# Optimization experiments

Measured on AMD Instinct MI355X. Metric: run time of the kernel, lower is better.

Reference implementation:

```python
import jax, jax.numpy as jnp
import numpy as np

B, S, E = 256, 128, 1024


def setup_inputs() -> dict:
    key = jax.random.key(0)
    k1, k2, k3, k4, k5 = jax.random.split(key, 5)
    x = jax.random.normal(k1, (B, S, E), dtype=jnp.float32)
    # ragged bags: start in [0,32), length in [1,96] so end <= 128 and bags are non-empty
    starts = jax.random.randint(k2, (B,), 0, 32)
    lengths = jax.random.randint(k3, (B,), 1, 97)
    document_index = jnp.stack([starts, starts + lengths], axis=-1).astype(jnp.int32)  # [B,2]
    scale = 1.0 / np.sqrt(E)
    W = jax.random.normal(k4, (E, E), dtype=jnp.float32) * scale  # relationMatrix.weight
    u = jax.random.normal(k5, (1, E), dtype=jnp.float32) * scale  # relationVector.weight
    return {"x": x, "W": W, "u": u, "document_index": document_index}


def reference(x, W, u, document_index):
    # scores_bs = relationVector(tanh(relationMatrix(x)))  (bias-free linears)
    h = jnp.tanh(jnp.einsum('bse,fe->bsf', x, W))          # [B,S,E]
    scores = jnp.einsum('bse,e->bs', h, u[0])              # [B,S]
    # ragged mask: position s belongs to doc b iff start <= s < end
    idx = jnp.arange(S)[None, :]                            # [1,S]
    mask = (idx >= document_index[:, :1]) & (idx < document_index[:, 1:])  # [B,S]
    attn = jax.nn.softmax(jnp.where(mask, scores, -jnp.inf), axis=-1)      # [B,S]
    attn = jnp.where(mask, attn, 0.0)
    out_concat = jnp.einsum('bs,bse->be', attn, x)          # [B,E]
    # keep_attention in the original is the last bag's softmax weights;
    # here returned padded to length S (zeros outside the bag)
    keep_attention = attn[-1]                               # [S]
    return out_concat, keep_attention
```

## Files before the change

kernel.cpp:

```cpp
#include <hip/hip_runtime.h>
#include <math.h>

#define Bb 256
#define Ss 128
#define Ee 1024
#define BK 64
#define APAD 72
#define NMAX 2048

typedef __bf16 bf16x8 __attribute__((ext_vector_type(8)));
typedef float f32x4 __attribute__((ext_vector_type(4)));

typedef __attribute__((address_space(3))) unsigned int lds_u32;
typedef __attribute__((address_space(1))) unsigned int glb_u32;

static __device__ __forceinline__ unsigned short f2bf(float f) {
    unsigned int u = __float_as_uint(f);
    u += 0x7FFFu + ((u >> 16) & 1u);
    return (unsigned short)(u >> 16);
}
static __device__ __forceinline__ float bf2f(unsigned short h) {
    return __uint_as_float((unsigned int)h << 16);
}

__global__ void build_list(const int* __restrict__ doc, int* __restrict__ list) {
    __shared__ int sc[256];
    const int b = threadIdx.x;
    const int start = doc[2 * b], end = doc[2 * b + 1];
    const int s0 = start >> 4;
    const int ns = ((end + 15) >> 4) - s0;
    sc[b] = ns;
    __syncthreads();
    for (int d = 1; d < 256; d <<= 1) {
        int v = sc[b];
        int add = (b >= d) ? sc[b - d] : 0;
        __syncthreads();
        sc[b] = v + add;
        __syncthreads();
    }
    const int total = sc[255];
    const int off = sc[b] - ns;
    for (int i = 0; i < ns; ++i)
        list[off + i] = b * Ss + ((s0 + i) << 4);
    for (int i = total + b; i < NMAX; i += 256)
        list[i] = -1;
}

__global__ void conv_all(const float* __restrict__ x,
                         const float* __restrict__ W,
                         const int* __restrict__ doc,
                         unsigned short* __restrict__ xb,
                         unsigned short* __restrict__ Wb) {
    const int st = blockIdx.x, by = blockIdx.y, tid = threadIdx.x;
    if (by >= Bb) {
        int i = ((((by - Bb) << 3) | st) << 8) | tid;
        float4 v = reinterpret_cast<const float4*>(W)[i];
        ushort4 o;
        o.x = f2bf(v.x); o.y = f2bf(v.y); o.z = f2bf(v.z); o.w = f2bf(v.w);
        reinterpret_cast<ushort4*>(Wb)[i] = o;
        return;
    }
    const int b = by;
    const int start = doc[2 * b], end = doc[2 * b + 1];
    const int strip0 = start >> 4;
    const int ns = ((end + 15) >> 4) - strip0;
    if (st < strip0 || st >= strip0 + ns) return;
    const size_t base = ((size_t)b * Ss + (st << 4)) * Ee;
    #pragma unroll
    for (int r = 0; r < 16; ++r) {
        size_t idx = base + (size_t)r * Ee + (tid << 2);
        float4 v = *reinterpret_cast<const float4*>(x + idx);
        ushort4 o;
        o.x = f2bf(v.x); o.y = f2bf(v.y); o.z = f2bf(v.z); o.w = f2bf(v.w);
        *reinterpret_cast<ushort4*>(xb + idx) = o;
    }
}

__global__ void convW_kernel(const float* __restrict__ W, unsigned short* __restrict__ Wb) {
    int i = blockIdx.x * blockDim.x + threadIdx.x;
    float4 v = reinterpret_cast<const float4*>(W)[i];
    ushort4 o;
    o.x = f2bf(v.x); o.y = f2bf(v.y); o.z = f2bf(v.z); o.w = f2bf(v.w);
    reinterpret_cast<ushort4*>(Wb)[i] = o;
}

__launch_bounds__(256, 6)
__global__ void scores_gemm_xb(const unsigned short* __restrict__ xb,
                               const unsigned short* __restrict__ Wb,
                               const float* __restrict__ u,
                               const int* __restrict__ list,
                               float* __restrict__ part) {
    __shared__ __align__(16) unsigned short As[64 * BK];
    __shared__ __align__(16) unsigned short Bs[128 * BK];
    __shared__ float s_red[4][64];

    const int mb = blockIdx.x;
    const int ft = blockIdx.y;

    int e0 = list[mb << 2];
    if (e0 < 0) return;
    int e[4];
    bool val[4];
    e[0] = e0; val[0] = true;
    #pragma unroll
    for (int j = 1; j < 4; ++j) {
        int v = list[(mb << 2) | j];
        val[j] = v >= 0;
        e[j] = val[j] ? v : e0;
    }

    const int tid  = threadIdx.x;
    const int wave = tid >> 6;
    const int lane = tid & 63;
    const int quad = lane >> 4;
    const int l16  = lane & 15;

    const unsigned short* wbase = Wb + (size_t)ft * 128 * Ee;

    f32x4 acc[4][2];
    #pragma unroll
    for (int i = 0; i < 4; ++i)
        #pragma unroll
        for (int j = 0; j < 2; ++j) acc[i][j] = (f32x4){0.f, 0.f, 0.f, 0.f};

    for (int t = 0; t < 16; ++t) {
        const int k0 = t << 6;
        #pragma unroll
        for (int r = 0; r < 2; ++r) {
            int chunk = (r << 8) | tid;
            int arow = chunk >> 3;
            int strip = arow >> 4;
            int rowin = arow & 15;
            int c8 = (chunk & 7) ^ (arow & 7);
            __builtin_amdgcn_global_load_lds(
                (const glb_u32*)(xb + ((size_t)e[strip] + rowin) * Ee + k0 + (c8 << 3)),
                (lds_u32*)&As[chunk << 3], 16, 0, 0);
        }
        #pragma unroll
        for (int r = 0; r < 4; ++r) {
            int chunk = (r << 8) | tid;
            int brow = chunk >> 3;
            int c8 = (chunk & 7) ^ (brow & 7);
            __builtin_amdgcn_global_load_lds(
                (const glb_u32*)(wbase + (size_t)brow * Ee + k0 + (c8 << 3)),
                (lds_u32*)&Bs[chunk << 3], 16, 0, 0);
        }
        __syncthreads();

        #pragma unroll
        for (int kk = 0; kk < BK; kk += 32) {
            const int n0 = wave * 32 + l16;
            const int n1 = n0 + 16;
            const int c8k = (kk >> 3) + quad;
            bf16x8 bf0 = *reinterpret_cast<const bf16x8*>(
                &Bs[((n0 << 3) | (c8k ^ (n0 & 7))) << 3]);
            bf16x8 bf1 = *reinterpret_cast<const bf16x8*>(
                &Bs[((n1 << 3) | (c8k ^ (n1 & 7))) << 3]);
            #pragma unroll
            for (int st = 0; st < 4; ++st) {
                const int ar = st * 16 + l16;
                bf16x8 af = *reinterpret_cast<const bf16x8*>(
                    &As[((ar << 3) | (c8k ^ (ar & 7))) << 3]);
                acc[st][0] = __builtin_amdgcn_mfma_f32_16x16x32_bf16(af, bf0, acc[st][0], 0, 0, 0);
                acc[st][1] = __builtin_amdgcn_mfma_f32_16x16x32_bf16(af, bf1, acc[st][1], 0, 0, 0);
            }
        }
        __syncthreads();
    }

    const float u0 = u[ft * 128 + wave * 32 + l16];
    const float u1 = u[ft * 128 + wave * 32 + 16 + l16];
    #pragma unroll
    for (int st = 0; st < 4; ++st) {
        float p[4];
        #pragma unroll
        for (int r = 0; r < 4; ++r)
            p[r] = tanhf(acc[st][0][r]) * u0 + tanhf(acc[st][1][r]) * u1;
        #pragma unroll
        for (int off = 8; off >= 1; off >>= 1)
            #pragma unroll
            for (int r = 0; r < 4; ++r)
                p[r] += __shfl_xor(p[r], off, 16);
        if (l16 == 0)
            #pragma unroll
            for (int r = 0; r < 4; ++r)
                s_red[wave][st * 16 + quad * 4 + r] = p[r];
    }
    __syncthreads();
    if (tid < 64) {
        const int strip = tid >> 4;
        if (val[strip]) {
            float v = s_red[0][tid] + s_red[1][tid] + s_red[2][tid] + s_red[3][tid];
            part[((size_t)(e[strip] + (tid & 15)) << 3) | ft] = v;
        }
    }
}

__launch_bounds__(256)
__global__ void scores_gemm_fb(const float* __restrict__ x,
                               const unsigned short* __restrict__ Wb,
                               const float* __restrict__ u,
                               const int* __restrict__ doc,
                               float* __restrict__ part) {
    __shared__ __align__(16) unsigned short As[8 * 16 * APAD];
    __shared__ __align__(16) unsigned short Bs[128 * BK];
    __shared__ float s_red[4][128];

    const int b  = blockIdx.x;
    const int ft = blockIdx.y;
    const int start = doc[2 * b], end = doc[2 * b + 1];
    const int strip0 = start >> 4;
    const int ns = ((end + 15) >> 4) - strip0;
    const int row0 = strip0 << 4;

    const int tid  = threadIdx.x;
    const int wave = tid >> 6;
    const int lane = tid & 63;
    const int quad = lane >> 4;
    const int l16  = lane & 15;
    const int arow = tid >> 4;
    const int acol = (tid & 15) << 2;

    const float* xbase = x + ((size_t)b * Ss + row0) * Ee;
    const unsigned short* wbase = Wb + (size_t)ft * 128 * Ee;

    f32x4 acc[8][2];
    #pragma unroll
    for (int i = 0; i < 8; ++i)
        #pragma unroll
        for (int j = 0; j < 2; ++j) acc[i][j] = (f32x4){0.f, 0.f, 0.f, 0.f};

    for (int k0 = 0; k0 < Ee; k0 += BK) {
        #pragma unroll
        for (int r = 0; r < 8; ++r) if (r < ns) {
            int row = (r << 4) | arow;
            float4 v = *reinterpret_cast<const float4*>(xbase + (size_t)row * Ee + k0 + acol);
            ushort4 o; o.x = f2bf(v.x); o.y = f2bf(v.y); o.z = f2bf(v.z); o.w = f2bf(v.w);
            *reinterpret_cast<ushort4*>(&As[row * APAD + acol]) = o;
        }
        #pragma unroll
        for (int r = 0; r < 4; ++r) {
            int chunk = (r << 8) | tid;
            int brow = chunk >> 3;
            int c8 = (chunk & 7) ^ (brow & 7);
            __builtin_amdgcn_global_load_lds(
                (const glb_u32*)(wbase + (size_t)brow * Ee + k0 + (c8 << 3)),
                (lds_u32*)&Bs[chunk << 3], 16, 0, 0);
        }
        __syncthreads();
        #pragma unroll
        for (int kk = 0; kk < BK; kk += 32) {
            const int n0 = wave * 32 + l16;
            const int n1 = n0 + 16;
            const int c8k = (kk >> 3) + quad;
            bf16x8 bf0 = *reinterpret_cast<const bf16x8*>(
                &Bs[((n0 << 3) | (c8k ^ (n0 & 7))) << 3]);
            bf16x8 bf1 = *reinterpret_cast<const bf16x8*>(
                &Bs[((n1 << 3) | (c8k ^ (n1 & 7))) << 3]);
            #pragma unroll
            for (int st = 0; st < 8; ++st) {
                if (st < ns) {
                    bf16x8 af = *reinterpret_cast<const bf16x8*>(
                        &As[(st * 16 + l16) * APAD + kk + quad * 8]);
                    acc[st][0] = __builtin_amdgcn_mfma_f32_16x16x32_bf16(af, bf0, acc[st][0], 0, 0, 0);
                    acc[st][1] = __builtin_amdgcn_mfma_f32_16x16x32_bf16(af, bf1, acc[st][1], 0, 0, 0);
                }
            }
        }
        __syncthreads();
    }

    const float u0 = u[ft * 128 + wave * 32 + l16];
    const float u1 = u[ft * 128 + wave * 32 + 16 + l16];
    #pragma unroll
    for (int st = 0; st < 8; ++st) {
        if (st < ns) {
            float p[4];
            #pragma unroll
            for (int r = 0; r < 4; ++r)
                p[r] = tanhf(acc[st][0][r]) * u0 + tanhf(acc[st][1][r]) * u1;
            #pragma unroll
            for (int off = 8; off >= 1; off >>= 1)
                #pragma unroll
                for (int r = 0; r < 4; ++r)
                    p[r] += __shfl_xor(p[r], off, 16);
            if (l16 == 0)
                #pragma unroll
                for (int r = 0; r < 4; ++r)
                    s_red[wave][st * 16 + quad * 4 + r] = p[r];
        }
    }
    __syncthreads();
    if (tid < (ns << 4)) {
        float v = s_red[0][tid] + s_red[1][tid] + s_red[2][tid] + s_red[3][tid];
        part[((size_t)(b * Ss + row0 + tid) << 3) | ft] = v;
    }
}

__global__ void out_fused(const unsigned short* __restrict__ xb,
                          const float* __restrict__ x,
                          const float* __restrict__ part,
                          const int* __restrict__ doc,
                          float* __restrict__ out,
                          float* __restrict__ keep) {
    const int c = blockIdx.x, b = blockIdx.y, t = threadIdx.x;
    const int start = doc[2 * b], end = doc[2 * b + 1];
    __shared__ float a_s[Ss];
    __shared__ float red[2];

    bool m = false;
    float sc = -INFINITY;
    if (t < Ss) {
        m = (t >= start) && (t < end);
        if (m) {
            const float4* p = reinterpret_cast<const float4*>(part + ((size_t)(b * Ss + t) << 3));
            float4 p0 = p[0], p1 = p[1];
            sc = ((p0.x + p0.y) + (p0.z + p0.w)) + ((p1.x + p1.y) + (p1.z + p1.w));
        }
    }
    float v = sc;
    #pragma unroll
    for (int off = 32; off >= 1; off >>= 1)
        v = fmaxf(v, __shfl_xor(v, off, 64));
    if (t < Ss && (t & 63) == 0) red[t >> 6] = v;
    __syncthreads();
    const float mx = fmaxf(red[0], red[1]);
    __syncthreads();
    const float e = m ? __expf(sc - mx) : 0.f;
    v = e;
    #pragma unroll
    for (int off = 32; off >= 1; off >>= 1)
        v += __shfl_xor(v, off, 64);
    if (t < Ss && (t & 63) == 0) red[t >> 6] = v;
    __syncthreads();
    if (t < Ss) a_s[t] = e / (red[0] + red[1]);
    __syncthreads();
    if (b == Bb - 1 && c == 0 && t < Ss) keep[t] = a_s[t];

    const int slo = max(start, c << 5), shi = min(end, (c << 5) + 32);
    if (slo >= shi) return;

    float4 accv = {0.f, 0.f, 0.f, 0.f};
    if (xb) {
        const unsigned short* xr = xb + (size_t)b * Ss * Ee;
        for (int s = slo; s < shi; ++s) {
            float a = a_s[s];
            ushort4 q = *reinterpret_cast<const ushort4*>(xr + (size_t)s * Ee + (t << 2));
            accv.x += a * bf2f(q.x); accv.y += a * bf2f(q.y);
            accv.z += a * bf2f(q.z); accv.w += a * bf2f(q.w);
        }
    } else {
        const float4* xr = reinterpret_cast<const float4*>(x + (size_t)b * Ss * Ee);
        for (int s = slo; s < shi; ++s) {
            float a = a_s[s];
            float4 q = xr[s * 256 + t];
            accv.x += a * q.x; accv.y += a * q.y;
            accv.z += a * q.z; accv.w += a * q.w;
        }
    }
    float* o = out + (size_t)b * Ee + (t << 2);
    atomicAdd(o + 0, accv.x);
    atomicAdd(o + 1, accv.y);
    atomicAdd(o + 2, accv.z);
    atomicAdd(o + 3, accv.w);
}

extern "C" void kernel_launch(void* const* d_in, const int* in_sizes, int n_in,
                              void* d_out, int out_size, void* d_ws, size_t ws_size,
                              hipStream_t stream) {
    const float* x  = (const float*)d_in[0];
    const float* W  = (const float*)d_in[1];
    const float* u  = (const float*)d_in[2];
    const int* doc  = (const int*)d_in[3];
    float* out = (float*)d_out;

    const size_t szWb   = (size_t)Ee * Ee * 2;
    const size_t szXb   = (size_t)Bb * Ss * Ee * 2;
    const size_t szPart = (size_t)Bb * Ss * 8 * 4;
    const size_t szList = (size_t)NMAX * 4;

    unsigned short* Wb = (unsigned short*)d_ws;
    const bool big_ws = ws_size >= szWb + szXb + szPart + szList;

    hipMemsetAsync(out, 0, (size_t)Bb * Ee * sizeof(float), stream);

    if (big_ws) {
        unsigned short* xbuf = (unsigned short*)((char*)d_ws + szWb);
        float* part = (float*)((char*)d_ws + szWb + szXb);
        int* list = (int*)((char*)d_ws + szWb + szXb + szPart);
        build_list<<<1, 256, 0, stream>>>(doc, list);
        conv_all<<<dim3(8, Bb + 128), 256, 0, stream>>>(x, W, doc, xbuf, Wb);
        scores_gemm_xb<<<dim3(NMAX / 4, 8), 256, 0, stream>>>(xbuf, Wb, u, list, part);
        out_fused<<<dim3(4, Bb), 256, 0, stream>>>(xbuf, x, part, doc, out, out + (size_t)Bb * Ee);
    } else {
        float* part = (float*)((char*)d_ws + szWb);
        convW_kernel<<<1024, 256, 0, stream>>>(W, Wb);
        scores_gemm_fb<<<dim3(Bb, 8), 256, 0, stream>>>(x, Wb, u, doc, part);
        out_fused<<<dim3(4, Bb), 256, 0, stream>>>(nullptr, x, part, doc, out, out + (size_t)Bb * Ee);
    }
}
```

Measured before the change: 261.4 us.

## Widen GEMM N-tile to 256, fold list build into conversion, drop atomics

The scores GEMM now computes 256 output features per block instead of 128, halving the grid's feature dimension and rereading each x tile half as often. The s_red scratch reuses the As buffer, and partial scores drop from 8 to 4 per row. The list-building kernel is merged into conv_all as an extra block, removing a launch. out_fused now splits work by column quarter instead of sequence chunk, reducing in shared memory and storing directly, which removes the memset and atomics. The wider tile raises register use and lowers the occupancy hint to 4, which may reduce latency hiding.

```diff
diff --git a/kernel.cpp b/kernel.cpp
--- a/kernel.cpp
+++ b/kernel.cpp
@@ -23,35 +23,37 @@
     return __uint_as_float((unsigned int)h << 16);
 }
 
-__global__ void build_list(const int* __restrict__ doc, int* __restrict__ list) {
-    __shared__ int sc[256];
-    const int b = threadIdx.x;
-    const int start = doc[2 * b], end = doc[2 * b + 1];
-    const int s0 = start >> 4;
-    const int ns = ((end + 15) >> 4) - s0;
-    sc[b] = ns;
-    __syncthreads();
-    for (int d = 1; d < 256; d <<= 1) {
-        int v = sc[b];
-        int add = (b >= d) ? sc[b - d] : 0;
-        __syncthreads();
-        sc[b] = v + add;
-        __syncthreads();
-    }
-    const int total = sc[255];
-    const int off = sc[b] - ns;
-    for (int i = 0; i < ns; ++i)
-        list[off + i] = b * Ss + ((s0 + i) << 4);
-    for (int i = total + b; i < NMAX; i += 256)
-        list[i] = -1;
-}
-
 __global__ void conv_all(const float* __restrict__ x,
                          const float* __restrict__ W,
                          const int* __restrict__ doc,
                          unsigned short* __restrict__ xb,
-                         unsigned short* __restrict__ Wb) {
+                         unsigned short* __restrict__ Wb,
+                         int* __restrict__ list) {
     const int st = blockIdx.x, by = blockIdx.y, tid = threadIdx.x;
+    if (by == Bb + 128) {
+        if (st != 0) return;
+        __shared__ int sc[256];
+        const int b = tid;
+        const int start = doc[2 * b], end = doc[2 * b + 1];
+        const int s0 = start >> 4;
+        const int ns = ((end + 15) >> 4) - s0;
+        sc[b] = ns;
+        __syncthreads();
+        for (int d = 1; d < 256; d <<= 1) {
+            int v = sc[b];
+            int add = (b >= d) ? sc[b - d] : 0;
+            __syncthreads();
+            sc[b] = v + add;
+            __syncthreads();
+        }
+        const int total = sc[255];
+        const int off = sc[b] - ns;
+        for (int i = 0; i < ns; ++i)
+            list[off + i] = b * Ss + ((s0 + i) << 4);
+        for (int i = total + b; i < NMAX; i += 256)
+            list[i] = -1;
+        return;
+    }
     if (by >= Bb) {
         int i = ((((by - Bb) << 3) | st) << 8) | tid;
         float4 v = reinterpret_cast<const float4*>(W)[i];
@@ -84,18 +86,17 @@
     reinterpret_cast<ushort4*>(Wb)[i] = o;
 }
 
-__launch_bounds__(256, 6)
+__launch_bounds__(256, 4)
 __global__ void scores_gemm_xb(const unsigned short* __restrict__ xb,
                                const unsigned short* __restrict__ Wb,
                                const float* __restrict__ u,
                                const int* __restrict__ list,
                                float* __restrict__ part) {
     __shared__ __align__(16) unsigned short As[64 * BK];
-    __shared__ __align__(16) unsigned short Bs[128 * BK];
-    __shared__ float s_red[4][64];
+    __shared__ __align__(16) unsigned short Bs[256 * BK];
 
     const int mb = blockIdx.x;
-    const int ft = blockIdx.y;
+    const int fg = blockIdx.y;
 
     int e0 = list[mb << 2];
     if (e0 < 0) return;
@@ -115,13 +116,13 @@
     const int quad = lane >> 4;
     const int l16  = lane & 15;
 
-    const unsigned short* wbase = Wb + (size_t)ft * 128 * Ee;
-
-    f32x4 acc[4][2];
+    const unsigned short* wbase = Wb + (size_t)(fg * 256) * Ee;
+
+    f32x4 acc[4][4];
     #pragma unroll
     for (int i = 0; i < 4; ++i)
         #pragma unroll
-        for (int j = 0; j < 2; ++j) acc[i][j] = (f32x4){0.f, 0.f, 0.f, 0.f};
+        for (int j = 0; j < 4; ++j) acc[i][j] = (f32x4){0.f, 0.f, 0.f, 0.f};
 
     for (int t = 0; t < 16; ++t) {
         const int k0 = t << 6;
@@ -129,15 +130,13 @@
         for (int r = 0; r < 2; ++r) {
             int chunk = (r << 8) | tid;
             int arow = chunk >> 3;
-            int strip = arow >> 4;
-            int rowin = arow & 15;
             int c8 = (chunk & 7) ^ (arow & 7);
             __builtin_amdgcn_global_load_lds(
-                (const glb_u32*)(xb + ((size_t)e[strip] + rowin) * Ee + k0 + (c8 << 3)),
+                (const glb_u32*)(xb + ((size_t)e[arow >> 4] + (arow & 15)) * Ee + k0 + (c8 << 3)),
                 (lds_u32*)&As[chunk << 3], 16, 0, 0);
         }
         #pragma unroll
-        for (int r = 0; r < 4; ++r) {
+        for (int r = 0; r < 8; ++r) {
             int chunk = (r << 8) | tid;
             int brow = chunk >> 3;
             int c8 = (chunk & 7) ^ (brow & 7);
@@ -149,33 +148,40 @@
 
         #pragma unroll
         for (int kk = 0; kk < BK; kk += 32) {
-            const int n0 = wave * 32 + l16;
-            const int n1 = n0 + 16;
             const int c8k = (kk >> 3) + quad;
-            bf16x8 bf0 = *reinterpret_cast<const bf16x8*>(
-                &Bs[((n0 << 3) | (c8k ^ (n0 & 7))) << 3]);
-            bf16x8 bf1 = *reinterpret_cast<const bf16x8*>(
-                &Bs[((n1 << 3) | (c8k ^ (n1 & 7))) << 3]);
+            bf16x8 bf[4];
+            #pragma unroll
+            for (int j = 0; j < 4; ++j) {
+                const int n = wave * 64 + j * 16 + l16;
+                bf[j] = *reinterpret_cast<const bf16x8*>(
+                    &Bs[((n << 3) | (c8k ^ (n & 7))) << 3]);
+            }
             #pragma unroll
             for (int st = 0; st < 4; ++st) {
                 const int ar = st * 16 + l16;
                 bf16x8 af = *reinterpret_cast<const bf16x8*>(
                     &As[((ar << 3) | (c8k ^ (ar & 7))) << 3]);
-                acc[st][0] = __builtin_amdgcn_mfma_f32_16x16x32_bf16(af, bf0, acc[st][0], 0, 0, 0);
-                acc[st][1] = __builtin_amdgcn_mfma_f32_16x16x32_bf16(af, bf1, acc[st][1], 0, 0, 0);
+                #pragma unroll
+                for (int j = 0; j < 4; ++j)
+                    acc[st][j] = __builtin_amdgcn_mfma_f32_16x16x32_bf16(af, bf[j], acc[st][j], 0, 0, 0);
             }
         }
         __syncthreads();
     }
 
-    const float u0 = u[ft * 128 + wave * 32 + l16];
-    const float u1 = u[ft * 128 + wave * 32 + 16 + l16];
+    float* s_red = reinterpret_cast<float*>(As);
+    float uj[4];
+    #pragma unroll
+    for (int j = 0; j < 4; ++j)
+        uj[j] = u[fg * 256 + wave * 64 + j * 16 + l16];
     #pragma unroll
     for (int st = 0; st < 4; ++st) {
         float p[4];
         #pragma unroll
-        for (int r = 0; r < 4; ++r)
-            p[r] = tanhf(acc[st][0][r]) * u0 + tanhf(acc[st][1][r]) * u1;
+        for (int r = 0; r < 4; ++r) {
+            p[r] = tanhf(acc[st][0][r]) * uj[0] + tanhf(acc[st][1][r]) * uj[1]
+                 + tanhf(acc[st][2][r]) * uj[2] + tanhf(acc[st][3][r]) * uj[3];
+        }
         #pragma unroll
         for (int off = 8; off >= 1; off >>= 1)
             #pragma unroll
@@ -184,14 +190,14 @@
         if (l16 == 0)
             #pragma unroll
             for (int r = 0; r < 4; ++r)
-                s_red[wave][st * 16 + quad * 4 + r] = p[r];
+                s_red[wave * 64 + st * 16 + quad * 4 + r] = p[r];
     }
     __syncthreads();
     if (tid < 64) {
         const int strip = tid >> 4;
         if (val[strip]) {
-            float v = s_red[0][tid] + s_red[1][tid] + s_red[2][tid] + s_red[3][tid];
-            part[((size_t)(e[strip] + (tid & 15)) << 3) | ft] = v;
+            float v = s_red[tid] + s_red[64 + tid] + s_red[128 + tid] + s_red[192 + tid];
+            part[(((size_t)e[strip] + (tid & 15)) << 2) | fg] = v;
         }
     }
 }
@@ -302,20 +308,26 @@
                           const float* __restrict__ part,
                           const int* __restrict__ doc,
                           float* __restrict__ out,
-                          float* __restrict__ keep) {
-    const int c = blockIdx.x, b = blockIdx.y, t = threadIdx.x;
+                          float* __restrict__ keep,
+                          int np8) {
+    const int h = blockIdx.x, b = blockIdx.y, t = threadIdx.x;
     const int start = doc[2 * b], end = doc[2 * b + 1];
     __shared__ float a_s[Ss];
     __shared__ float red[2];
+    __shared__ float4 red4[4][64];
 
     bool m = false;
     float sc = -INFINITY;
     if (t < Ss) {
         m = (t >= start) && (t < end);
         if (m) {
-            const float4* p = reinterpret_cast<const float4*>(part + ((size_t)(b * Ss + t) << 3));
-            float4 p0 = p[0], p1 = p[1];
-            sc = ((p0.x + p0.y) + (p0.z + p0.w)) + ((p1.x + p1.y) + (p1.z + p1.w));
+            const float* pp = part + (size_t)(b * Ss + t) * (np8 ? 8 : 4);
+            float4 p0 = *reinterpret_cast<const float4*>(pp);
+            sc = (p0.x + p0.y) + (p0.z + p0.w);
+            if (np8) {
+                float4 p1 = *reinterpret_cast<const float4*>(pp + 4);
+                sc += (p1.x + p1.y) + (p1.z + p1.w);
+            }
         }
     }
     float v = sc;
@@ -335,34 +347,38 @@
     __syncthreads();
     if (t < Ss) a_s[t] = e / (red[0] + red[1]);
     __syncthreads();
-    if (b == Bb - 1 && c == 0 && t < Ss) keep[t] = a_s[t];
-
-    const int slo = max(start, c << 5), shi = min(end, (c << 5) + 32);
-    if (slo >= shi) return;
-
+    if (h == 0 && b == Bb - 1 && t < Ss) keep[t] = a_s[t];
+
+    const int ssub = t >> 6, tt = t & 63;
     float4 accv = {0.f, 0.f, 0.f, 0.f};
     if (xb) {
-        const unsigned short* xr = xb + (size_t)b * Ss * Ee;
-        for (int s = slo; s < shi; ++s) {
+        const unsigned short* xr = xb + (size_t)b * Ss * Ee + h * 256 + (tt << 2);
+        for (int s = start + ssub; s < end; s += 4) {
             float a = a_s[s];
-            ushort4 q = *reinterpret_cast<const ushort4*>(xr + (size_t)s * Ee + (t << 2));
+            ushort4 q = *reinterpret_cast<const ushort4*>(xr + (size_t)s * Ee);
             accv.x += a * bf2f(q.x); accv.y += a * bf2f(q.y);
             accv.z += a * bf2f(q.z); accv.w += a * bf2f(q.w);
         }
     } else {
-        const float4* xr = reinterpret_cast<const float4*>(x + (size_t)b * Ss * Ee);
-        for (int s = slo; s < shi; ++s) {
+        const float* xr = x + (size_t)b * Ss * Ee + h * 256 + (tt << 2);
+        for (int s = start + ssub; s < end; s += 4) {
             float a = a_s[s];
-            float4 q = xr[s * 256 + t];
+            float4 q = *reinterpret_cast<const float4*>(xr + (size_t)s * Ee);
             accv.x += a * q.x; accv.y += a * q.y;
             accv.z += a * q.z; accv.w += a * q.w;
         }
     }
-    float* o = out + (size_t)b * Ee + (t << 2);
-    atomicAdd(o + 0, accv.x);
-    atomicAdd(o + 1, accv.y);
-    atomicAdd(o + 2, accv.z);
-    atomicAdd(o + 3, accv.w);
+    red4[ssub][tt] = accv;
+    __syncthreads();
+    if (t < 64) {
+        float4 r0 = red4[0][t], r1 = red4[1][t], r2 = red4[2][t], r3 = red4[3][t];
+        float4 s;
+        s.x = (r0.x + r1.x) + (r2.x + r3.x);
+        s.y = (r0.y + r1.y) + (r2.y + r3.y);
+        s.z = (r0.z + r1.z) + (r2.z + r3.z);
+        s.w = (r0.w + r1.w) + (r2.w + r3.w);
+        reinterpret_cast<float4*>(out + (size_t)b * Ee + h * 256)[t] = s;
+    }
 }
 
 extern "C" void kernel_launch(void* const* d_in, const int* in_sizes, int n_in,
@@ -382,20 +398,17 @@
     unsigned short* Wb = (unsigned short*)d_ws;
     const bool big_ws = ws_size >= szWb + szXb + szPart + szList;
 
-    hipMemsetAsync(out, 0, (size_t)Bb * Ee * sizeof(float), stream);
-
     if (big_ws) {
         unsigned short* xbuf = (unsigned short*)((char*)d_ws + szWb);
         float* part = (float*)((char*)d_ws + szWb + szXb);
         int* list = (int*)((char*)d_ws + szWb + szXb + szPart);
-        build_list<<<1, 256, 0, stream>>>(doc, list);
-        conv_all<<<dim3(8, Bb + 128), 256, 0, stream>>>(x, W, doc, xbuf, Wb);
-        scores_gemm_xb<<<dim3(NMAX / 4, 8), 256, 0, stream>>>(xbuf, Wb, u, list, part);
-        out_fused<<<dim3(4, Bb), 256, 0, stream>>>(xbuf, x, part, doc, out, out + (size_t)Bb * Ee);
+        conv_all<<<dim3(8, Bb + 129), 256, 0, stream>>>(x, W, doc, xbuf, Wb, list);
+        scores_gemm_xb<<<dim3(NMAX / 4, 4), 256, 0, stream>>>(xbuf, Wb, u, list, part);
+        out_fused<<<dim3(4, Bb), 256, 0, stream>>>(xbuf, x, part, doc, out, out + (size_t)Bb * Ee, 0);
     } else {
         float* part = (float*)((char*)d_ws + szWb);
         convW_kernel<<<1024, 256, 0, stream>>>(W, Wb);
         scores_gemm_fb<<<dim3(Bb, 8), 256, 0, stream>>>(x, Wb, u, doc, part);
-        out_fused<<<dim3(4, Bb), 256, 0, stream>>>(nullptr, x, part, doc, out, out + (size_t)Bb * Ee);
-    }
-}
+        out_fused<<<dim3(4, Bb), 256, 0, stream>>>(nullptr, x, part, doc, out, out + (size_t)Bb * Ee, 1);
+    }
+}
```

Measured after the change: 245.6 us. 1.06x faster.
